# Kernel tuning notes

Hardware: AMD Instinct MI355X
Metric: run time of the kernel (lower is better)

The kernel has to match this reference:

```python
import jax, jax.numpy as jnp
import numpy as np

EPS = 1e-6

def _ln2d(x, w, b):
    # LayerNorm2d: normalize over channel dim per pixel
    mu = x.mean(axis=1, keepdims=True)
    var = ((x - mu) ** 2).mean(axis=1, keepdims=True)
    return (x - mu) / jnp.sqrt(var + EPS) * w[None, :, None, None] + b[None, :, None, None]

def _conv1x1(x, w, b):
    return jnp.einsum('oc,bchw->bohw', w, x) + b[None, :, None, None]

def setup_inputs() -> dict:
    key = jax.random.key(0)
    ks = jax.random.split(key, 20)
    B, c, H, W = 4, 32, 256, 256
    dw = 2 * c
    k, wH, wW = 3, 32, 32
    s = 0.05
    d = {}
    d['inp'] = jax.random.normal(ks[0], (B, c, H, W), jnp.float32)
    d['conv2_weight'] = jax.random.normal(ks[1], (B, dw, k, k, wH, wW), jnp.float32) * 0.1
    d['conv1_w'] = jax.random.normal(ks[2], (dw, c), jnp.float32) * s
    d['conv1_b'] = jnp.zeros((dw,), jnp.float32)
    d['conv3_w'] = jax.random.normal(ks[3], (c, c), jnp.float32) * s
    d['conv3_b'] = jnp.zeros((c,), jnp.float32)
    d['sca_w'] = jax.random.normal(ks[4], (c, c), jnp.float32) * s
    d['sca_b'] = jnp.zeros((c,), jnp.float32)
    d['conv4_w'] = jax.random.normal(ks[5], (dw, c), jnp.float32) * s
    d['conv4_b'] = jnp.zeros((dw,), jnp.float32)
    d['conv5_w'] = jax.random.normal(ks[6], (c, c), jnp.float32) * s
    d['conv5_b'] = jnp.zeros((c,), jnp.float32)
    d['norm1_w'] = jnp.ones((c,), jnp.float32)
    d['norm1_b'] = jnp.zeros((c,), jnp.float32)
    d['norm2_w'] = jnp.ones((c,), jnp.float32)
    d['norm2_b'] = jnp.zeros((c,), jnp.float32)
    # original inits these to zero; use small random so the block is non-trivial
    d['beta'] = jax.random.normal(ks[7], (1, c, 1, 1), jnp.float32) * 0.1
    d['gamma'] = jax.random.normal(ks[8], (1, c, 1, 1), jnp.float32) * 0.1
    return d

def reference(inp, conv2_weight, conv1_w, conv1_b, conv3_w, conv3_b, sca_w, sca_b,
              conv4_w, conv4_b, conv5_w, conv5_b, norm1_w, norm1_b, norm2_w, norm2_b,
              beta, gamma):
    B, c, H, W = inp.shape
    x = _ln2d(inp, norm1_w, norm1_b)
    x = _conv1x1(x, conv1_w, conv1_b)                 # [B, 2c, H, W]
    Bw, C, kH, kW, wH, wW = conv2_weight.shape
    # bilinear upsample (half-pixel centers, == torch align_corners=False)
    w2 = conv2_weight.reshape(B * C, kH * kW, wH, wW)
    w2 = jax.image.resize(w2, (B * C, kH * kW, H, W), method='linear')
    w2 = w2.reshape(B, C, kH * kW, H, W)
    # ddf with all-ones channel filter + 'mul' == per-pixel spatial 3x3 conv per channel
    pad = kH // 2
    xp = jnp.pad(x, ((0, 0), (0, 0), (pad, pad), (pad, pad)))
    patches = jnp.stack([xp[:, :, i:i + H, j:j + W]
                         for i in range(kH) for j in range(kW)], axis=2)  # [B,2c,9,H,W]
    x = (patches * w2).sum(axis=2)                    # [B, 2c, H, W]
    x1, x2 = jnp.split(x, 2, axis=1)                  # SimpleGate
    x = x1 * x2                                       # [B, c, H, W]
    s = _conv1x1(x.mean(axis=(2, 3), keepdims=True), sca_w, sca_b)
    x = x * s
    x = _conv1x1(x, conv3_w, conv3_b)
    y = inp + x * beta
    x = _conv1x1(_ln2d(y, norm2_w, norm2_b), conv4_w, conv4_b)
    x1, x2 = jnp.split(x, 2, axis=1)
    x = _conv1x1(x1 * x2, conv5_w, conv5_b)
    return y + x * gamma
```

## Files before the change

kernel.cpp:

```cpp
#include <hip/hip_runtime.h>
#include <hip/hip_bf16.h>

typedef __hip_bfloat16 bf16;
typedef __attribute__((ext_vector_type(8))) unsigned short u16x8;
typedef __attribute__((ext_vector_type(8))) short s16x8;
typedef __attribute__((ext_vector_type(4))) float f32x4;
typedef __attribute__((ext_vector_type(4))) unsigned short us16x4;

#define B_   4
#define C_   32
#define DW_  64
#define H_   256
#define W_   256
#define P_   65536
#define SRC_ 32
#define TRS_ 272
#define TPL_ 70176

#define OW1    0
#define OB1    2048
#define OW3    2112
#define OB3    3136
#define OWS    3168
#define OBS    4192
#define OW4    4224
#define OB4    6272
#define OW5    6336
#define OB5    7360
#define ON1W   7392
#define ON1B   7424
#define ON2W   7456
#define ON2B   7488
#define OBETA  7520
#define OGAMMA 7552
#define OSUMS  7584
#define OSVEC  7712
#define OFLAG  7900
#define CWF_BOFF 32768ull
#define T1_BOFF  (CWF_BOFF + 9437184ull)
#define G_BOFF   (T1_BOFF + 35930112ull)

__device__ __forceinline__ bf16  f2b(float v){ return __float2bfloat16(v); }
__device__ __forceinline__ float bfu(unsigned short u){ return __uint_as_float(((unsigned int)u) << 16); }
__device__ __forceinline__ unsigned short fbits(float v){
    bf16 b = __float2bfloat16(v);
    return *reinterpret_cast<unsigned short*>(&b);
}

template<typename T> __device__ __forceinline__ float ldf(const T* p);
template<> __device__ __forceinline__ float ldf<float>(const float* p){ return *p; }
template<> __device__ __forceinline__ float ldf<bf16>(const bf16* p){ return __bfloat162float(*p); }

template<typename T> __device__ __forceinline__ void stf(T* p, float v);
template<> __device__ __forceinline__ void stf<float>(float* p, float v){ *p = v; }
template<> __device__ __forceinline__ void stf<bf16>(bf16* p, float v){ *p = __float2bfloat16(v); }

template<typename T> struct dtag;
template<> struct dtag<float>{ static constexpr int v = 0; };
template<> struct dtag<bf16>{ static constexpr int v = 1; };

__device__ __forceinline__ f32x4 MF(s16x8 a, s16x8 b, f32x4 c){
    return __builtin_amdgcn_mfma_f32_16x16x32_bf16(a, b, c, 0, 0, 0);
}
__device__ __forceinline__ s16x8 wfrag8(const float* p){
    float4 a = *(const float4*)p;
    float4 c = *(const float4*)(p + 4);
    s16x8 r;
    r[0] = (short)fbits(a.x); r[1] = (short)fbits(a.y);
    r[2] = (short)fbits(a.z); r[3] = (short)fbits(a.w);
    r[4] = (short)fbits(c.x); r[5] = (short)fbits(c.y);
    r[6] = (short)fbits(c.z); r[7] = (short)fbits(c.w);
    return r;
}

__global__ void k_detect(const unsigned short* __restrict__ raw, int* __restrict__ flag)
{
    int t = threadIdx.x;
    int bad = 0;
    for (int k = 0; k < 8; ++k) {
        unsigned short u = raw[2 * (t + 64 * k)];
        float v = __uint_as_float(((unsigned int)u) << 16);
        if (!(fabsf(v) < 1e6f)) bad = 1;
    }
    int anybad = __any(bad);
    if (t == 0) *flag = anybad ? 0 : 1;
}

template<typename T>
__global__ void k_prep(const T* __restrict__ w1, const T* __restrict__ b1,
                       const T* __restrict__ w3, const T* __restrict__ b3,
                       const T* __restrict__ wsc, const T* __restrict__ bsc_,
                       const T* __restrict__ w4, const T* __restrict__ b4,
                       const T* __restrict__ w5, const T* __restrict__ b5,
                       const T* __restrict__ n1w, const T* __restrict__ n1b,
                       const T* __restrict__ n2w, const T* __restrict__ n2b,
                       const T* __restrict__ bet, const T* __restrict__ gam,
                       float* __restrict__ wsf, const int* __restrict__ flag)
{
    if (*flag != dtag<T>::v) return;
    int t = threadIdx.x;
    for (int i = t; i < 2048; i += 256) wsf[OW1 + i] = ldf<T>(w1 + i);
    for (int i = t; i < 64;   i += 256) wsf[OB1 + i] = ldf<T>(b1 + i);
    for (int i = t; i < 1024; i += 256) wsf[OW3 + i] = ldf<T>(w3 + i);
    for (int i = t; i < 32;   i += 256) wsf[OB3 + i] = ldf<T>(b3 + i);
    for (int i = t; i < 1024; i += 256) wsf[OWS + i] = ldf<T>(wsc + i);
    for (int i = t; i < 32;   i += 256) wsf[OBS + i] = ldf<T>(bsc_ + i);
    for (int i = t; i < 2048; i += 256) wsf[OW4 + i] = ldf<T>(w4 + i);
    for (int i = t; i < 64;   i += 256) wsf[OB4 + i] = ldf<T>(b4 + i);
    for (int i = t; i < 1024; i += 256) wsf[OW5 + i] = ldf<T>(w5 + i);
    for (int i = t; i < 32;   i += 256) wsf[OB5 + i] = ldf<T>(b5 + i);
    for (int i = t; i < 32;   i += 256) wsf[ON1W + i] = ldf<T>(n1w + i);
    for (int i = t; i < 32;   i += 256) wsf[ON1B + i] = ldf<T>(n1b + i);
    for (int i = t; i < 32;   i += 256) wsf[ON2W + i] = ldf<T>(n2w + i);
    for (int i = t; i < 32;   i += 256) wsf[ON2B + i] = ldf<T>(n2b + i);
    for (int i = t; i < 32;   i += 256) wsf[OBETA + i] = ldf<T>(bet + i);
    for (int i = t; i < 32;   i += 256) wsf[OGAMMA + i] = ldf<T>(gam + i);
    for (int i = t; i < 128;  i += 256) wsf[OSUMS + i] = 0.f;
}

__global__ void k_cwf(const void* __restrict__ cw, float4* __restrict__ cwf4,
                      const int* __restrict__ flag)
{
    int i4 = blockIdx.x * 256 + threadIdx.x;
    if (*flag == 0) {
        cwf4[i4] = ((const float4*)cw)[i4];
    } else {
        const ushort4* p = (const ushort4*)cw;
        ushort4 v = p[i4];
        cwf4[i4] = make_float4(bfu(v.x), bfu(v.y), bfu(v.z), bfu(v.w));
    }
}

__global__ void k_zpad(unsigned short* __restrict__ t1u)
{
    unsigned short* pl = t1u + (size_t)blockIdx.x * TPL_;
    int t = threadIdx.x;
    for (int i = t; i < 258; i += 256) {
        pl[i] = 0;
        pl[257 * TRS_ + i] = 0;
    }
    pl[(t + 1) * TRS_] = 0;
    pl[(t + 1) * TRS_ + 257] = 0;
}

template<typename T>
__device__ __forceinline__ void ln1_body(const T* __restrict__ inp,
        const float* __restrict__ wsf, bf16* __restrict__ t1p)
{
    int tid = blockIdx.x * 256 + threadIdx.x;
    int b = tid >> 16;
    int p = tid & 65535;
    int h = p >> 8, w = p & 255;
    const T* ip = inp + (size_t)b * C_ * P_ + p;
    float v[C_];
    float m = 0.f;
    #pragma unroll
    for (int ch = 0; ch < C_; ++ch) { v[ch] = ldf<T>(ip + ch * P_); m += v[ch]; }
    m *= (1.f / C_);
    float var = 0.f;
    #pragma unroll
    for (int ch = 0; ch < C_; ++ch) { float d = v[ch] - m; var += d * d; }
    var *= (1.f / C_);
    float inv = rsqrtf(var + 1e-6f);
    #pragma unroll
    for (int ch = 0; ch < C_; ++ch)
        v[ch] = (v[ch] - m) * inv * wsf[ON1W + ch] + wsf[ON1B + ch];

    bf16* op = t1p + (size_t)(b * DW_) * TPL_ + (h + 1) * TRS_ + (w + 1);
    #pragma unroll 4
    for (int o = 0; o < DW_; ++o) {
        float acc = wsf[OB1 + o];
        #pragma unroll
        for (int ch = 0; ch < C_; ++ch) acc += v[ch] * wsf[OW1 + o * C_ + ch];
        op[(size_t)o * TPL_] = f2b(acc);
    }
}

__global__ __launch_bounds__(256) void k_ln1_conv1(const void* __restrict__ inp,
        const float* __restrict__ wsf, bf16* __restrict__ t1p,
        const int* __restrict__ flag)
{
    if (*flag == 0) ln1_body<float>((const float*)inp, wsf, t1p);
    else            ln1_body<bf16>((const bf16*)inp, wsf, t1p);
}

#define G_ 4
__global__ __launch_bounds__(256, 4) void k_ddf(const unsigned short* __restrict__ t1u,
        const float* __restrict__ cwf, bf16* __restrict__ g, float* __restrict__ sums)
{
    __shared__ float CWs[4320];

    int bid = blockIdx.x;
    int tile = bid & 31;
    int cg  = (bid >> 5) & 7;
    int b   = bid >> 8;
    int th = tile >> 2, tw = tile & 3;
    int cellh0 = th * 4;
    int cellw0 = tw * 8;
    int cp0 = cg * G_;

    {
        const float* cb = cwf + (size_t)b * (DW_ * 9 * 1024);
        for (int it = 0; it < 17; ++it) {
            int idx = it * 256 + threadIdx.x;
            if (idx < 4320) {
                int cc  = idx % 10;
                int t2  = idx / 10;
                int rr  = t2 % 6;
                int t3  = t2 / 6;
                int tap = t3 % 9;
                int chl = t3 / 9;
                int ch = (chl < G_) ? (cp0 + chl) : (C_ + cp0 + chl - G_);
                int cr = cellh0 - 1 + rr; cr = cr < 0 ? 0 : (cr > 31 ? 31 : cr);
                int cw = cellw0 - 1 + cc; cw = cw < 0 ? 0 : (cw > 31 ? 31 : cw);
                CWs[idx] = cb[ch * 9216 + tap * 1024 + cr * SRC_ + cw];
            }
        }
    }
    __syncthreads();

    int lane = threadIdx.x & 63, wid = threadIdx.x >> 6;
    int k = lane >> 3, r = lane & 7;
    int cellh = cellh0 + wid;
    int h = cellh * 8 + r;
    int w = (cellw0 + k) * 8;

    int rsel = r >> 2;
    float fh = rsel ? ((float)r * 0.125f - 0.4375f) : ((float)r * 0.125f + 0.5625f);
    float gh = 1.f - fh;
    int rr0k = (wid + rsel) * 10 + k;

    const unsigned short* tb = t1u + (size_t)(b * DW_) * TPL_ + (size_t)h * TRS_ + w;
    bf16* gp = g + (size_t)(b * C_) * P_ + h * 256 + w;

    for (int l = 0; l < G_; ++l) {
        int cp = cp0 + l;
        const unsigned short* pl1 = tb + (size_t)cp * TPL_;
        const unsigned short* pl2 = pl1 + (size_t)C_ * TPL_;
        const float* q1 = CWs + l * 540;
        const float* q2 = CWs + (G_ + l) * 540;

        float acc1[8], acc2[8];
        #pragma unroll
        for (int pass = 0; pass < 2; ++pass) {
            const unsigned short* pl = pass ? pl2 : pl1;
            const float* q = pass ? q2 : q1;
            float* acc = pass ? acc2 : acc1;

            u16x8 v8[3];
            unsigned int ve[3];
            #pragma unroll
            for (int i = 0; i < 3; ++i) {
                const unsigned short* rp = pl + i * TRS_;
                v8[i] = *(const u16x8*)rp;
                ve[i] = *(const unsigned int*)(rp + 8);
            }
            float S00[8], S01[8], S10[8], S11[8];
            #pragma unroll
            for (int c = 0; c < 8; ++c) { S00[c]=0.f; S01[c]=0.f; S10[c]=0.f; S11[c]=0.f; }
            #pragma unroll
            for (int i = 0; i < 3; ++i) {
                float p[10];
                #pragma unroll
                for (int j = 0; j < 8; ++j) p[j] = bfu((unsigned short)v8[i][j]);
                p[8] = bfu((unsigned short)(ve[i] & 0xFFFFu));
                p[9] = bfu((unsigned short)(ve[i] >> 16));
                #pragma unroll
                for (int j = 0; j < 3; ++j) {
                    const float* qb = q + (i * 3 + j) * 60 + rr0k;
                    float w00 = qb[0],  w01 = qb[1],  w02 = qb[2];
                    float w10 = qb[10], w11 = qb[11], w12 = qb[12];
                    #pragma unroll
                    for (int c = 0; c < 8; ++c) {
                        float pv = p[c + j];
                        S00[c] += pv * ((c < 4) ? w00 : w01);
                        S01[c] += pv * ((c < 4) ? w01 : w02);
                        S10[c] += pv * ((c < 4) ? w10 : w11);
                        S11[c] += pv * ((c < 4) ? w11 : w12);
                    }
                }
            }
            const float fwt[8] = {0.5625f, 0.6875f, 0.8125f, 0.9375f,
                                  0.0625f, 0.1875f, 0.3125f, 0.4375f};
            #pragma unroll
            for (int c = 0; c < 8; ++c) {
                float fw = fwt[c], gw = 1.f - fw;
                acc[c] = gh * (gw * S00[c] + fw * S01[c]) + fh * (gw * S10[c] + fw * S11[c]);
            }
        }

        u16x8 ov;
        float s = 0.f;
        #pragma unroll
        for (int c = 0; c < 8; ++c) {
            float gv = acc1[c] * acc2[c];
            s += gv;
            bf16 bv = f2b(gv);
            ov[c] = *reinterpret_cast<unsigned short*>(&bv);
        }
        *(u16x8*)(gp + (size_t)cp * P_) = ov;

        #pragma unroll
        for (int off = 32; off >= 1; off >>= 1) s += __shfl_xor(s, off, 64);
        if (lane == 0) atomicAdd(&sums[b * C_ + cp], s);
    }
}

__global__ void k_sca(float* __restrict__ wsf)
{
    int t = threadIdx.x;
    int b = t >> 5, o = t & 31;
    float acc = wsf[OBS + o];
    #pragma unroll
    for (int ch = 0; ch < C_; ++ch)
        acc += wsf[OWS + o * C_ + ch] * (wsf[OSUMS + b * C_ + ch] * (1.f / (float)P_));
    wsf[OSVEC + b * C_ + o] = acc;
}

#define XSTR_ 32
#define ISTR_ 33

template<typename T>
__device__ __forceinline__ void tail_body(const T* __restrict__ inp,
        const bf16* __restrict__ g, const float* __restrict__ wsf,
        T* __restrict__ out, short* __restrict__ xsh, float* __restrict__ ipsh)
{
    const int t = threadIdx.x;
    const int b = blockIdx.x >> 8;
    const int p0 = (blockIdx.x & 255) << 8;

    {
        float sv[32];
        #pragma unroll
        for (int q = 0; q < 8; ++q) {
            float4 v = *(const float4*)(wsf + OSVEC + b * 32 + q * 4);
            sv[4*q+0] = v.x; sv[4*q+1] = v.y; sv[4*q+2] = v.z; sv[4*q+3] = v.w;
        }
        const unsigned short* gp = (const unsigned short*)g + (size_t)(b * C_) * P_ + p0 + t;
        unsigned short row[32];
        #pragma unroll
        for (int ch = 0; ch < C_; ++ch)
            row[ch] = fbits(bfu(gp[(size_t)ch * P_]) * sv[ch]);
        u16x8* xr = (u16x8*)(xsh + t * XSTR_);
        #pragma unroll
        for (int qq = 0; qq < 4; ++qq) {
            u16x8 vv;
            #pragma unroll
            for (int j = 0; j < 8; ++j) vv[j] = row[qq * 8 + j];
            xr[qq] = vv;
        }
        const T* ip = inp + (size_t)(b * C_) * P_ + p0 + t;
        float* ir = ipsh + t * ISTR_;
        #pragma unroll
        for (int ch = 0; ch < C_; ++ch)
            ir[ch] = ldf<T>(ip + (size_t)ch * P_);
    }
    __syncthreads();

    const int lane = t & 63, wv = t >> 6;
    const int l15 = lane & 15, l4 = lane >> 4;
    const int wp0 = wv * 64;

    s16x8 w3f[2], w4f[4];
    #pragma unroll
    for (int m = 0; m < 2; ++m) w3f[m] = wfrag8(wsf + OW3 + (m * 16 + l15) * 32 + l4 * 8);
    #pragma unroll
    for (int m = 0; m < 4; ++m) w4f[m] = wfrag8(wsf + OW4 + (m * 16 + l15) * 32 + l4 * 8);

    f32x4 y[2][4];
    {
        f32x4 b3v[2], btv[2];
        #pragma unroll
        for (int m = 0; m < 2; ++m) {
            b3v[m] = *(const f32x4*)(wsf + OB3   + m * 16 + l4 * 4);
            btv[m] = *(const f32x4*)(wsf + OBETA + m * 16 + l4 * 4);
        }
        #pragma unroll
        for (int tn = 0; tn < 4; ++tn) {
            int px = wp0 + tn * 16 + l15;
            s16x8 xb = *(const s16x8*)(xsh + px * XSTR_ + l4 * 8);
            const float* irr = ipsh + px * ISTR_ + l4 * 4;
            #pragma unroll
            for (int m = 0; m < 2; ++m) {
                f32x4 acc = MF(w3f[m], xb, b3v[m]);
                f32x4 yy;
                #pragma unroll
                for (int i = 0; i < 4; ++i)
                    yy[i] = irr[m * 16 + i] + acc[i] * btv[m][i];
                y[m][tn] = yy;
            }
        }
    }

    {
        f32x4 nwv[2], nbv[2];
        #pragma unroll
        for (int m = 0; m < 2; ++m) {
            nwv[m] = *(const f32x4*)(wsf + ON2W + m * 16 + l4 * 4);
            nbv[m] = *(const f32x4*)(wsf + ON2B + m * 16 + l4 * 4);
        }
        #pragma unroll
        for (int tn = 0; tn < 4; ++tn) {
            float s = 0.f;
            #pragma unroll
            for (int m = 0; m < 2; ++m)
                #pragma unroll
                for (int i = 0; i < 4; ++i) s += y[m][tn][i];
            s += __shfl_xor(s, 16);
            s += __shfl_xor(s, 32);
            float mean = s * (1.f / 32.f);
            float q = 0.f;
            #pragma unroll
            for (int m = 0; m < 2; ++m)
                #pragma unroll
                for (int i = 0; i < 4; ++i) { float d = y[m][tn][i] - mean; q += d * d; }
            q += __shfl_xor(q, 16);
            q += __shfl_xor(q, 32);
            float inv = rsqrtf(q * (1.f / 32.f) + 1e-6f);
            int px = wp0 + tn * 16 + l15;
            #pragma unroll
            for (int m = 0; m < 2; ++m) {
                us16x4 pk;
                #pragma unroll
                for (int i = 0; i < 4; ++i)
                    pk[i] = fbits((y[m][tn][i] - mean) * inv * nwv[m][i] + nbv[m][i]);
                *(us16x4*)(xsh + px * XSTR_ + m * 16 + l4 * 4) = pk;
            }
        }
    }

    {
        f32x4 b4v[4];
        #pragma unroll
        for (int m = 0; m < 4; ++m)
            b4v[m] = *(const f32x4*)(wsf + OB4 + m * 16 + l4 * 4);
        s16x8 yb[4];
        #pragma unroll
        for (int tn = 0; tn < 4; ++tn)
            yb[tn] = *(const s16x8*)(xsh + (wp0 + tn * 16 + l15) * XSTR_ + l4 * 8);
        #pragma unroll
        for (int tn = 0; tn < 4; ++tn) {
            f32x4 a4[4];
            #pragma unroll
            for (int m = 0; m < 4; ++m) a4[m] = MF(w4f[m], yb[tn], b4v[m]);
            int px = wp0 + tn * 16 + l15;
            #pragma unroll
            for (int m = 0; m < 2; ++m) {
                us16x4 pk;
                #pragma unroll
                for (int i = 0; i < 4; ++i) pk[i] = fbits(a4[m][i] * a4[m + 2][i]);
                *(us16x4*)(xsh + px * XSTR_ + m * 16 + l4 * 4) = pk;
            }
        }
    }

    {
        s16x8 w5f[2];
        #pragma unroll
        for (int m = 0; m < 2; ++m) w5f[m] = wfrag8(wsf + OW5 + (m * 16 + l15) * 32 + l4 * 8);
        f32x4 b5v[2], gmv[2];
        #pragma unroll
        for (int m = 0; m < 2; ++m) {
            b5v[m] = *(const f32x4*)(wsf + OB5    + m * 16 + l4 * 4);
            gmv[m] = *(const f32x4*)(wsf + OGAMMA + m * 16 + l4 * 4);
        }
        s16x8 ub[4];
        #pragma unroll
        for (int tn = 0; tn < 4; ++tn)
            ub[tn] = *(const s16x8*)(xsh + (wp0 + tn * 16 + l15) * XSTR_ + l4 * 8);
        #pragma unroll
        for (int tn = 0; tn < 4; ++tn) {
            int px = p0 + wp0 + tn * 16 + l15;
            #pragma unroll
            for (int m = 0; m < 2; ++m) {
                f32x4 acc = MF(w5f[m], ub[tn], b5v[m]);
                #pragma unroll
                for (int i = 0; i < 4; ++i) {
                    int och = m * 16 + l4 * 4 + i;
                    stf<T>(out + (size_t)(b * C_ + och) * P_ + px,
                           y[m][tn][i] + acc[i] * gmv[m][i]);
                }
            }
        }
    }
}

__global__ __launch_bounds__(256, 3) void k_tail(const void* __restrict__ inp,
        const bf16* __restrict__ g, const float* __restrict__ wsf,
        void* __restrict__ out, const int* __restrict__ flag)
{
    __shared__ short xsh[256 * XSTR_];
    __shared__ float ipsh[256 * ISTR_];
    if (*flag == 0) tail_body<float>((const float*)inp, g, wsf, (float*)out, xsh, ipsh);
    else            tail_body<bf16>((const bf16*)inp, g, wsf, (bf16*)out, xsh, ipsh);
}

extern "C" void kernel_launch(void* const* d_in, const int* in_sizes, int n_in,
                              void* d_out, int out_size, void* d_ws, size_t ws_size,
                              hipStream_t stream)
{
    float* wsf = (float*)d_ws;
    char* wsb = (char*)d_ws;
    float* cwf = (float*)(wsb + CWF_BOFF);
    bf16* t1p = (bf16*)(wsb + T1_BOFF);
    bf16* g   = (bf16*)(wsb + G_BOFF);
    int* flag = (int*)(wsf + OFLAG);

    k_detect<<<1, 64, 0, stream>>>((const unsigned short*)d_in[0], flag);

    int nblk = (B_ * P_) / 256;

    k_prep<float><<<1, 256, 0, stream>>>(
        (const float*)d_in[2], (const float*)d_in[3], (const float*)d_in[4],
        (const float*)d_in[5], (const float*)d_in[6], (const float*)d_in[7],
        (const float*)d_in[8], (const float*)d_in[9], (const float*)d_in[10],
        (const float*)d_in[11], (const float*)d_in[12], (const float*)d_in[13],
        (const float*)d_in[14], (const float*)d_in[15], (const float*)d_in[16],
        (const float*)d_in[17], wsf, flag);
    k_prep<bf16><<<1, 256, 0, stream>>>(
        (const bf16*)d_in[2], (const bf16*)d_in[3], (const bf16*)d_in[4],
        (const bf16*)d_in[5], (const bf16*)d_in[6], (const bf16*)d_in[7],
        (const bf16*)d_in[8], (const bf16*)d_in[9], (const bf16*)d_in[10],
        (const bf16*)d_in[11], (const bf16*)d_in[12], (const bf16*)d_in[13],
        (const bf16*)d_in[14], (const bf16*)d_in[15], (const bf16*)d_in[16],
        (const bf16*)d_in[17], wsf, flag);

    k_cwf<<<2304, 256, 0, stream>>>(d_in[1], (float4*)cwf, flag);

    k_zpad<<<256, 256, 0, stream>>>((unsigned short*)t1p);

    k_ln1_conv1<<<nblk, 256, 0, stream>>>(d_in[0], wsf, t1p, flag);

    k_ddf<<<1024, 256, 0, stream>>>((const unsigned short*)t1p, cwf, g, wsf + OSUMS);

    k_sca<<<1, 128, 0, stream>>>(wsf);

    k_tail<<<nblk, 256, 0, stream>>>(d_in[0], g, wsf, d_out, flag);
}
```

Baseline: 266.0 us.

## Use MFMA for LN1 conv1 and halve DDF channel group size

The LN1+conv1 kernel now writes the normalized pixels into shared memory as bf16 and computes the 64x32 1x1 conv with MFMA instructions rather than a scalar per-thread FMA loop. Separately, the DDF kernel drops from 4 to 2 channels per block, which doubles the grid, halves shared memory, and raises the launch-bounds occupancy hint. The aim is to remove the scalar FMA cost in conv1 and improve occupancy in DDF. The costs are an extra bf16 rounding of the normalized input, a scattered store pattern from the MFMA output layout, and more redundant filter loads in DDF.

```diff
diff --git a/kernel.cpp b/kernel.cpp
--- a/kernel.cpp
+++ b/kernel.cpp
@@ -145,55 +145,87 @@
 
 template<typename T>
 __device__ __forceinline__ void ln1_body(const T* __restrict__ inp,
-        const float* __restrict__ wsf, bf16* __restrict__ t1p)
-{
-    int tid = blockIdx.x * 256 + threadIdx.x;
-    int b = tid >> 16;
-    int p = tid & 65535;
-    int h = p >> 8, w = p & 255;
-    const T* ip = inp + (size_t)b * C_ * P_ + p;
-    float v[C_];
-    float m = 0.f;
+        const float* __restrict__ wsf, bf16* __restrict__ t1p, short* __restrict__ xsh)
+{
+    const int t = threadIdx.x;
+    const int b = blockIdx.x >> 8;
+    const int p0 = (blockIdx.x & 255) << 8;
+
+    {
+        const T* ip = inp + (size_t)(b * C_) * P_ + p0 + t;
+        float v[C_];
+        float m = 0.f;
+        #pragma unroll
+        for (int ch = 0; ch < C_; ++ch) { v[ch] = ldf<T>(ip + (size_t)ch * P_); m += v[ch]; }
+        m *= (1.f / C_);
+        float var = 0.f;
+        #pragma unroll
+        for (int ch = 0; ch < C_; ++ch) { float d = v[ch] - m; var += d * d; }
+        var *= (1.f / C_);
+        float inv = rsqrtf(var + 1e-6f);
+        u16x8* xr = (u16x8*)(xsh + t * 32);
+        #pragma unroll
+        for (int qq = 0; qq < 4; ++qq) {
+            u16x8 vv;
+            #pragma unroll
+            for (int j = 0; j < 8; ++j) {
+                int ch = qq * 8 + j;
+                vv[j] = fbits((v[ch] - m) * inv * wsf[ON1W + ch] + wsf[ON1B + ch]);
+            }
+            xr[qq] = vv;
+        }
+    }
+    __syncthreads();
+
+    const int lane = t & 63, wv = t >> 6;
+    const int l15 = lane & 15, l4 = lane >> 4;
+    const int wp0 = wv * 64;
+
+    s16x8 w1f[4];
+    f32x4 b1v[4];
     #pragma unroll
-    for (int ch = 0; ch < C_; ++ch) { v[ch] = ldf<T>(ip + ch * P_); m += v[ch]; }
-    m *= (1.f / C_);
-    float var = 0.f;
+    for (int m = 0; m < 4; ++m) {
+        w1f[m] = wfrag8(wsf + OW1 + (m * 16 + l15) * 32 + l4 * 8);
+        b1v[m] = *(const f32x4*)(wsf + OB1 + m * 16 + l4 * 4);
+    }
+
+    const int h = p0 >> 8;
+    bf16* op = t1p + (size_t)(b * DW_) * TPL_ + (size_t)(h + 1) * TRS_ + 1;
     #pragma unroll
-    for (int ch = 0; ch < C_; ++ch) { float d = v[ch] - m; var += d * d; }
-    var *= (1.f / C_);
-    float inv = rsqrtf(var + 1e-6f);
-    #pragma unroll
-    for (int ch = 0; ch < C_; ++ch)
-        v[ch] = (v[ch] - m) * inv * wsf[ON1W + ch] + wsf[ON1B + ch];
-
-    bf16* op = t1p + (size_t)(b * DW_) * TPL_ + (h + 1) * TRS_ + (w + 1);
-    #pragma unroll 4
-    for (int o = 0; o < DW_; ++o) {
-        float acc = wsf[OB1 + o];
-        #pragma unroll
-        for (int ch = 0; ch < C_; ++ch) acc += v[ch] * wsf[OW1 + o * C_ + ch];
-        op[(size_t)o * TPL_] = f2b(acc);
-    }
-}
-
-__global__ __launch_bounds__(256) void k_ln1_conv1(const void* __restrict__ inp,
+    for (int tn = 0; tn < 4; ++tn) {
+        int px = wp0 + tn * 16 + l15;
+        s16x8 xb = *(const s16x8*)(xsh + px * 32 + l4 * 8);
+        #pragma unroll
+        for (int m = 0; m < 4; ++m) {
+            f32x4 acc = MF(w1f[m], xb, b1v[m]);
+            #pragma unroll
+            for (int i = 0; i < 4; ++i) {
+                int och = m * 16 + l4 * 4 + i;
+                op[(size_t)och * TPL_ + px] = f2b(acc[i]);
+            }
+        }
+    }
+}
+
+__global__ __launch_bounds__(256, 4) void k_ln1_conv1(const void* __restrict__ inp,
         const float* __restrict__ wsf, bf16* __restrict__ t1p,
         const int* __restrict__ flag)
 {
-    if (*flag == 0) ln1_body<float>((const float*)inp, wsf, t1p);
-    else            ln1_body<bf16>((const bf16*)inp, wsf, t1p);
-}
-
-#define G_ 4
-__global__ __launch_bounds__(256, 4) void k_ddf(const unsigned short* __restrict__ t1u,
+    __shared__ short xsh[256 * 32];
+    if (*flag == 0) ln1_body<float>((const float*)inp, wsf, t1p, xsh);
+    else            ln1_body<bf16>((const bf16*)inp, wsf, t1p, xsh);
+}
+
+#define G_ 2
+__global__ __launch_bounds__(256, 8) void k_ddf(const unsigned short* __restrict__ t1u,
         const float* __restrict__ cwf, bf16* __restrict__ g, float* __restrict__ sums)
 {
-    __shared__ float CWs[4320];
+    __shared__ float CWs[2160];
 
     int bid = blockIdx.x;
     int tile = bid & 31;
-    int cg  = (bid >> 5) & 7;
-    int b   = bid >> 8;
+    int cg  = (bid >> 5) & 15;
+    int b   = bid >> 9;
     int th = tile >> 2, tw = tile & 3;
     int cellh0 = th * 4;
     int cellw0 = tw * 8;
@@ -201,9 +233,9 @@
 
     {
         const float* cb = cwf + (size_t)b * (DW_ * 9 * 1024);
-        for (int it = 0; it < 17; ++it) {
+        for (int it = 0; it < 9; ++it) {
             int idx = it * 256 + threadIdx.x;
-            if (idx < 4320) {
+            if (idx < 2160) {
                 int cc  = idx % 10;
                 int t2  = idx / 10;
                 int rr  = t2 % 6;
@@ -531,7 +563,7 @@
 
     k_ln1_conv1<<<nblk, 256, 0, stream>>>(d_in[0], wsf, t1p, flag);
 
-    k_ddf<<<1024, 256, 0, stream>>>((const unsigned short*)t1p, cwf, g, wsf + OSUMS);
+    k_ddf<<<2048, 256, 0, stream>>>((const unsigned short*)t1p, cwf, g, wsf + OSUMS);
 
     k_sca<<<1, 128, 0, stream>>>(wsf);
 
```

Measured after the change: 401.0 us. 1.51x slower.
